# Kernel tuning notes

Hardware: AMD Instinct MI355X
Metric: run time of the kernel (lower is better)

The kernel has to match this reference:

```python
import jax, jax.numpy as jnp
import numpy as np

C_LOGIT = 10.0  # logit clipping constant C from __init__
NEG_INF = -1e9


def setup_inputs() -> dict:
    key = jax.random.key(0)
    ks = jax.random.split(key, 12)
    B, S, E, H = 128, 1024, 128, 128
    sE = 1.0 / np.sqrt(E)
    s2E = 1.0 / np.sqrt(2 * E)
    return {
        "node_context": jnp.zeros((1,), jnp.float32),   # unused: low-decoder results are discarded
        "original_data": jnp.zeros((1,), jnp.float32),  # unused
        "cell_context": jax.random.normal(ks[0], (B, S, E), jnp.float32),
        "high_mask": jnp.zeros((B, S), jnp.float32),
        "low_mask": jnp.zeros((1,), jnp.float32),       # unused
        # learned parameters
        "init_w": jax.random.uniform(ks[1], (2 * E,), jnp.float32, -1.0, 1.0),
        "Wc": jax.random.uniform(ks[2], (E, E), jnp.float32, -sE, sE),    # h_context_embed
        "bc": jax.random.uniform(ks[3], (E,), jnp.float32, -sE, sE),
        "Wv": jax.random.uniform(ks[4], (2 * E, E), jnp.float32, -s2E, s2E),  # v_weight_embed
        "bv": jax.random.uniform(ks[5], (E,), jnp.float32, -s2E, s2E),
        "W_ref": jax.random.uniform(ks[6], (E, H), jnp.float32, -sE, sE),  # pointer target proj
        "W_q": jax.random.uniform(ks[7], (E, H), jnp.float32, -sE, sE),    # pointer query proj
        "v": jax.random.uniform(ks[8], (H,), jnp.float32, -1.0 / np.sqrt(H), 1.0 / np.sqrt(H)),
    }


def reference(node_context, original_data, cell_context, high_mask, low_mask,
              init_w, Wc, bc, Wv, bv, W_ref, W_q, v):
    B, S, E = cell_context.shape
    h_bar = jnp.mean(cell_context, axis=1) @ Wc + bc            # [B, E]
    ref = jnp.einsum('bse,eh->bsh', cell_context, W_ref)        # [B, S, H] (loop-invariant)
    q0 = h_bar + (init_w @ Wv + bv)                             # [B, E]
    mask0 = high_mask.at[:, 0].set(1.0)                         # start node masked
    base_key = jax.random.key(42)

    def step(carry, i):
        query, mask, init_h = carry
        q = query @ W_q                                         # [B, H]
        u = C_LOGIT * jnp.tanh(jnp.einsum('bsh,h->bs', jnp.tanh(ref + q[:, None, :]), v))
        logits = jnp.where(mask > 0, NEG_INF, u)                # [B, S]
        k = jax.random.fold_in(base_key, i)
        idx = jax.random.categorical(k, logits)                 # [B] sampled next node
        logp = jnp.take_along_axis(jax.nn.log_softmax(logits, -1), idx[:, None], 1)[:, 0]
        mask = mask.at[jnp.arange(B), idx].set(1.0)             # Environment.update_state
        h = jnp.take_along_axis(cell_context, idx[:, None, None], 1)[:, 0, :]  # gather emb
        init_h = jnp.where(i == 0, h, init_h)                   # frozen after first step
        query = h_bar + jnp.concatenate([init_h, h], axis=-1) @ Wv + bv
        return (query, mask, init_h), (logp, idx)

    init = (q0, mask0, jnp.zeros((B, E), cell_context.dtype))
    _, (logps, idxs) = jax.lax.scan(step, init, jnp.arange(S - 1))
    # original returns (stack(log_probs, 1), stack(idx, 1))
    return logps.T, idxs.T
```

## Files before the change

### kernel.cpp

```cpp
#include <hip/hip_runtime.h>
#include <hip/hip_bf16.h>
#include <stdint.h>

#pragma clang fp contract(off)

#define Bn 128
#define Sn 1024
#define En 128
#define NSTEP 1023
#define REQ_WS ((size_t)Bn * 128 * Sn * 4)

__device__ __forceinline__ uint2 threefry2x32(uint32_t k0, uint32_t k1,
                                              uint32_t x0, uint32_t x1) {
  uint32_t ks2 = k0 ^ k1 ^ 0x1BD11BDAu;
  x0 += k0; x1 += k1;
#define TFR(r) { x0 += x1; x1 = (x1 << (r)) | (x1 >> (32 - (r))); x1 ^= x0; }
  TFR(13) TFR(15) TFR(26) TFR(6)
  x0 += k1;  x1 += ks2 + 1u;
  TFR(17) TFR(29) TFR(16) TFR(24)
  x0 += ks2; x1 += k0 + 2u;
  TFR(13) TFR(15) TFR(26) TFR(6)
  x0 += k0;  x1 += k1 + 3u;
  TFR(17) TFR(29) TFR(16) TFR(24)
  x0 += k1;  x1 += ks2 + 4u;
  TFR(13) TFR(15) TFR(26) TFR(6)
  x0 += ks2; x1 += k0 + 5u;
#undef TFR
  return make_uint2(x0, x1);
}

__device__ __forceinline__ float xla_tanh(float x) {
#pragma clang fp contract(off)
  float cx = fmaxf(-7.90531110763549805f, fminf(x, 7.90531110763549805f));
  float x2 = cx * cx;
  float nu = -2.76076847742355e-16f;
  nu = x2 * nu + 2.00018790482477e-13f;
  nu = x2 * nu + -8.60467152213735e-11f;
  nu = x2 * nu + 5.12229709037114e-08f;
  nu = x2 * nu + 1.48572235717979e-05f;
  nu = x2 * nu + 6.37261928875436e-04f;
  nu = x2 * nu + 4.89352455891786e-03f;
  nu = cx * nu;
  float de = 1.19825839466702e-06f;
  de = x2 * de + 1.18534705686654e-04f;
  de = x2 * de + 2.26843463243900e-03f;
  de = x2 * de + 4.89352518554385e-03f;
  float r = nu / de;
  return (fabsf(x) < 0.0004f) ? x : r;
}

__device__ __forceinline__ float cephes_logf(float x) {
#pragma clang fp contract(off)
  uint32_t ix = __float_as_uint(x);
  int e = (int)(ix >> 23) - 126;
  float m = __uint_as_float((ix & 0x007FFFFFu) | 0x3F000000u);
  if (m < 0.70710678118654752440f) { e -= 1; m = m + m; }
  float xm = m - 1.0f;
  float z = xm * xm;
  float y = 7.0376836292e-2f;
  y = y * xm + -1.1514610310e-1f;
  y = y * xm + 1.1676998740e-1f;
  y = y * xm + -1.2420140846e-1f;
  y = y * xm + 1.4249322787e-1f;
  y = y * xm + -1.6668057665e-1f;
  y = y * xm + 2.0000714765e-1f;
  y = y * xm + -2.4999993993e-1f;
  y = y * xm + 3.3333331174e-1f;
  y = y * xm;
  y = y * z;
  float fe = (float)e;
  y = y + fe * -2.12194440e-4f;
  y = y - 0.5f * z;
  float res = xm + y;
  res = res + fe * 0.693359375f;
  return res;
}

__device__ __forceinline__ float cephes_expf(float x) {
#pragma clang fp contract(off)
  x = fminf(fmaxf(x, -88.3762626647949f), 88.3762626647950f);
  float fx = x * 1.44269504088896341f + 0.5f;
  fx = floorf(fx);
  x = x - fx * 0.693359375f;
  x = x - fx * -2.12194440e-4f;
  float z = x * x;
  float y = 1.9875691500e-4f;
  y = y * x + 1.3981999507e-3f;
  y = y * x + 8.3334519073e-3f;
  y = y * x + 4.1665795894e-2f;
  y = y * x + 1.6666665459e-1f;
  y = y * x + 5.0000001201e-1f;
  y = y * z + x;
  y = y + 1.0f;
  return ldexpf(y, (int)fx);
}

__device__ __forceinline__ uint32_t f32_orderable(float f) {
  uint32_t b = __float_as_uint(f);
  return (b & 0x80000000u) ? ~b : (b | 0x80000000u);
}

__global__ void k_mark(float* out, float val) { out[0] = val; }

__global__ __launch_bounds__(256) void k_ref(const float* __restrict__ cc,
    const float* __restrict__ W_ref, float* __restrict__ refT) {
#pragma clang fp contract(off)
  int b = blockIdx.y, s0 = blockIdx.x * 128, t = threadIdx.x;
  __shared__ float tile[128 * 129];
  const float* src = cc + ((size_t)b * Sn + s0) * En;
  for (int i = t; i < 128 * 128; i += 256) {
    int sl = i >> 7, e = i & 127;
    tile[sl * 129 + e] = src[i];
  }
  __syncthreads();
  for (int i = t; i < 128 * 128; i += 256) {
    int sl = i >> 7, h = i & 127;
    float acc = 0.0f;
    for (int e = 0; e < En; ++e)
      acc = acc + tile[sl * 129 + e] * W_ref[e * 128 + h];
    refT[((size_t)b * Sn + (s0 + sl)) * 128 + h] = acc;
  }
}

__global__ __launch_bounds__(1024) void k_decode(
    const float* __restrict__ cc, const float* __restrict__ high_mask,
    const float* __restrict__ init_w, const float* __restrict__ Wc,
    const float* __restrict__ bc, const float* __restrict__ Wv,
    const float* __restrict__ bv, const float* __restrict__ W_q,
    const float* __restrict__ v, const float* __restrict__ refT,
    float* __restrict__ out, int half) {
#pragma clang fp contract(off)
  const int b = blockIdx.x, tid = threadIdx.x;
  const int lane = tid & 63, wid = tid >> 6;
  const int hsel = tid & 1;
  const int row1 = tid >> 1;
  __shared__ __align__(16) float wq_s[128 * 128];
  __shared__ __align__(16) float wvhi_s[128 * 128];
  __shared__ __align__(16) float mean_s[128], q_s[128], query_s[128], hbar_s[128];
  __shared__ __align__(16) float v_s[128], bv_s[128], cvec[256], dlow_s[128];
  __shared__ float uv[1024];
  __shared__ unsigned short list2[2][1024];
  __shared__ unsigned long long wkey[16];
  __shared__ float wsum[16];
  __shared__ int n_s;
  __shared__ uint32_t key_s[2];

  for (int j = tid; j < 128 * 128; j += 1024) wq_s[j] = W_q[j];
  for (int j = tid; j < 128 * 128; j += 1024) wvhi_s[j] = Wv[128 * 128 + j];
  if (tid < 128) {
    float acc = 0.0f;
    const float* base = cc + (size_t)b * Sn * En + tid;
    for (int s = 0; s < Sn; ++s) acc = acc + base[(size_t)s * En];
    mean_s[tid] = acc / 1024.0f;
  }
  if (tid == 512) {
    int n = 0;
    for (int s = 0; s < Sn; ++s) {
      bool masked = (s == 0) || (high_mask[(size_t)b * Sn + s] > 0.0f);
      if (!masked) list2[0][n++] = (unsigned short)s;
    }
    n_s = n;
  }
  __syncthreads();
  if (tid < 128) {
    float hb = 0.0f;
    for (int e = 0; e < 128; ++e) hb = hb + mean_s[e] * Wc[e * 128 + tid];
    hb = hb + bc[tid];
    float wd = 0.0f;
    for (int k = 0; k < 256; ++k) wd = wd + init_w[k] * Wv[k * 128 + tid];
    wd = wd + bv[tid];
    hbar_s[tid] = hb;
    query_s[tid] = hb + wd;
    v_s[tid] = v[tid];
    bv_s[tid] = bv[tid];
  }
  __syncthreads();
  const int n0 = n_s;

  const float* refb = refT + (size_t)b * Sn * 128;
  const float4* q4 = (const float4*)q_s;
  const float4* v4 = (const float4*)v_s;

  for (int i = 0; i < NSTEP; ++i) {
    const int n = n0 - i;
    const unsigned short* lcur = list2[i & 1];
    unsigned short* lnxt = list2[(i + 1) & 1];

    if (tid < 128) {
      float acc = 0.0f;
#pragma unroll 8
      for (int k = 0; k < 128; ++k) acc = acc + query_s[k] * wq_s[k * 128 + tid];
      q_s[tid] = acc;
    } else if (tid == 512) {
      uint2 kk2 = threefry2x32(0u, 42u, 0u, (uint32_t)i);
      key_s[0] = kk2.x; key_s[1] = kk2.y;
    }
    __syncthreads();

    const int npass = (2 * n + 1023) >> 10;
    unsigned long long kk = 0ull;
    float ee = 0.0f;
    for (int pass = 0; pass < npass; ++pass) {
      const int row = (pass << 9) + row1;
      if (row < n) {
        const int s = lcur[row];
        const float4* rb4 = (const float4*)(refb + (size_t)s * 128);
        float4 rA[8];
#pragma unroll
        for (int j = 0; j < 8; ++j) rA[j] = rb4[2 * j + hsel];
        float a0 = 0.f, a1 = 0.f, a2 = 0.f, a3 = 0.f;
        float4 rB[8];
#pragma unroll
        for (int c2 = 0; c2 < 8; ++c2) {
          rB[c2] = rb4[2 * (c2 + 8) + hsel];
          const float4 qv = q4[2 * c2 + hsel];
          const float4 vv = v4[2 * c2 + hsel];
          const float4 r = rA[c2];
          a0 = a0 + xla_tanh(r.x + qv.x) * vv.x;
          a1 = a1 + xla_tanh(r.y + qv.y) * vv.y;
          a2 = a2 + xla_tanh(r.z + qv.z) * vv.z;
          a3 = a3 + xla_tanh(r.w + qv.w) * vv.w;
        }
#pragma unroll
        for (int c2 = 8; c2 < 16; ++c2) {
          const float4 qv = q4[2 * c2 + hsel];
          const float4 vv = v4[2 * c2 + hsel];
          const float4 r = rB[c2 - 8];
          a0 = a0 + xla_tanh(r.x + qv.x) * vv.x;
          a1 = a1 + xla_tanh(r.y + qv.y) * vv.y;
          a2 = a2 + xla_tanh(r.z + qv.z) * vv.z;
          a3 = a3 + xla_tanh(r.w + qv.w) * vv.w;
        }
        float o0 = __shfl_xor(a0, 1, 64), o1 = __shfl_xor(a1, 1, 64);
        float o2 = __shfl_xor(a2, 1, 64), o3 = __shfl_xor(a3, 1, 64);
        if (hsel == 0) {
          float h0 = a0 + o0, h1 = a1 + o1, h2 = a2 + o2, h3 = a3 + o3;
          float dot = (h0 + h2) + (h1 + h3);
          float u = 10.0f * xla_tanh(dot);
          uint32_t f = (uint32_t)(b * Sn + s);
          uint2 hh = threefry2x32(key_s[0], key_s[1], 0u, f);
          uint32_t bits = hh.x ^ hh.y;
          float uf = __uint_as_float((bits >> 9) | 0x3F800000u) - 1.0f;
          uf = uf + 1.17549435e-38f;
          uf = fmaxf(1.17549435e-38f, uf);
          float g = -cephes_logf(-cephes_logf(uf));
          float y = u + g;
          uv[row] = u;
          unsigned long long k2 =
              ((unsigned long long)f32_orderable(y) << 32) | (uint32_t)(0xFFFFFFFFu - (uint32_t)row);
          if (k2 > kk) kk = k2;
          ee = ee + cephes_expf(u);
        }
      }
    }
    for (int off = 32; off >= 1; off >>= 1) {
      unsigned long long o = __shfl_xor(kk, off, 64);
      if (o > kk) kk = o;
      ee = ee + __shfl_xor(ee, off, 64);
    }
    if (lane == 0) { wkey[wid] = kk; wsum[wid] = ee; }
    __syncthreads();

    unsigned long long km = wkey[0];
    float es = wsum[0];
    for (int w = 1; w < 16; ++w) {
      if (wkey[w] > km) km = wkey[w];
      es = es + wsum[w];
    }
    int p = (int)(0xFFFFFFFFu - (uint32_t)(km & 0xFFFFFFFFu));
    p = (p >= 0 && p < 1024) ? p : 0;
    const int idx = lcur[p];
    if (tid < 128) {
      float hval = cc[((size_t)b * Sn + idx) * En + tid];
      cvec[128 + tid] = hval;
      if (i == 0) cvec[tid] = hval;
    }
    if (tid < n - 1) lnxt[tid] = lcur[tid + (tid >= p ? 1 : 0)];
    if (tid == 0) {
      float logp = uv[p] - cephes_logf(es);
      out[(size_t)b * NSTEP + i] = logp;
      out[(size_t)half + (size_t)b * NSTEP + i] = (float)idx;
    }
    __syncthreads();

    if (tid < 128) {
      float d;
      if (i == 0) {
        float dl = 0.0f;
#pragma unroll 8
        for (int k = 0; k < 128; ++k) dl = dl + cvec[k] * Wv[k * 128 + tid];
        dlow_s[tid] = dl;
        d = dl;
      } else {
        d = dlow_s[tid];
      }
#pragma unroll 8
      for (int k = 0; k < 128; ++k) d = d + cvec[128 + k] * wvhi_s[k * 128 + tid];
      query_s[tid] = (hbar_s[tid] + d) + bv_s[tid];
    }
    __syncthreads();
  }
}

extern "C" void kernel_launch(void* const* d_in, const int* in_sizes, int n_in,
                              void* d_out, int out_size, void* d_ws, size_t ws_size,
                              hipStream_t stream) {
  const float* cc     = (const float*)d_in[2];
  const float* hm     = (const float*)d_in[3];
  const float* init_w = (const float*)d_in[5];
  const float* Wc     = (const float*)d_in[6];
  const float* bc     = (const float*)d_in[7];
  const float* Wv     = (const float*)d_in[8];
  const float* bv     = (const float*)d_in[9];
  const float* W_ref  = (const float*)d_in[10];
  const float* W_q    = (const float*)d_in[11];
  const float* v      = (const float*)d_in[12];
  float* out = (float*)d_out;

  if (ws_size < REQ_WS) {
    float mib = (float)(ws_size >> 20);
    hipLaunchKernelGGL(k_mark, dim3(1), dim3(1), 0, stream, out, 100000.0f * (mib + 1.0f));
    return;
  }

  float* refT = (float*)d_ws;
  const int half = out_size / 2;

  hipLaunchKernelGGL(k_ref, dim3(Sn / 128, Bn), dim3(256), 0, stream, cc, W_ref, refT);
  hipLaunchKernelGGL(k_decode, dim3(Bn), dim3(1024), 0, stream,
                     cc, hm, init_w, Wc, bc, Wv, bv, W_q, v, refT, out, half);
}
```

Baseline: 22.43 ms.

## Split each batch row's decode across two workgroups with global-memory handshake

```diff
diff --git a/kernel.cpp b/kernel.cpp
--- a/kernel.cpp
+++ b/kernel.cpp
@@ -9,6 +9,8 @@
 #define En 128
 #define NSTEP 1023
 #define REQ_WS ((size_t)Bn * 128 * Sn * 4)
+#define XCH_BYTES 5120
+#define REQ_WS2 (REQ_WS + (size_t)8192)
 
 __device__ __forceinline__ uint2 threefry2x32(uint32_t k0, uint32_t k1,
                                               uint32_t x0, uint32_t x1) {
@@ -102,6 +104,8 @@
 
 __global__ void k_mark(float* out, float val) { out[0] = val; }
 
+__global__ void k_zero(unsigned int* p) { p[blockIdx.x * 256 + threadIdx.x] = 0u; }
+
 __global__ __launch_bounds__(256) void k_ref(const float* __restrict__ cc,
     const float* __restrict__ W_ref, float* __restrict__ refT) {
 #pragma clang fp contract(off)
@@ -122,7 +126,204 @@
   }
 }
 
-__global__ __launch_bounds__(1024) void k_decode(
+__global__ __launch_bounds__(1024) void k_decode2(
+    const float* __restrict__ cc, const float* __restrict__ high_mask,
+    const float* __restrict__ init_w, const float* __restrict__ Wc,
+    const float* __restrict__ bc, const float* __restrict__ Wv,
+    const float* __restrict__ bv, const float* __restrict__ W_q,
+    const float* __restrict__ v, const float* __restrict__ refT,
+    float* __restrict__ out, int half, void* xbase) {
+#pragma clang fp contract(off)
+  const int b = blockIdx.x >> 1, side = blockIdx.x & 1, tid = threadIdx.x;
+  const int lane = tid & 63, wid = tid >> 6;
+  const int hsel = tid & 1;
+  unsigned long long* xk = (unsigned long long*)xbase;
+  float* xe = (float*)((char*)xbase + 2048);
+  float* xu = (float*)((char*)xbase + 3072);
+  uint32_t* xf = (uint32_t*)((char*)xbase + 4096);
+  const int me = (b << 1) | side, other = me ^ 1;
+
+  __shared__ __align__(16) float wq_s[128 * 128];
+  __shared__ __align__(16) float wvhi_s[128 * 128];
+  __shared__ __align__(16) float mean_s[128], q_s[128], query_s[128], hbar_s[128];
+  __shared__ __align__(16) float v_s[128], bv_s[128], cvec[256], dlow_s[128];
+  __shared__ float uv[1024];
+  __shared__ unsigned short list2[2][1024];
+  __shared__ unsigned long long wkey[16];
+  __shared__ float wsum[16];
+  __shared__ int n_s, p_ls;
+  __shared__ float up_ls, es_ls;
+  __shared__ uint32_t key_s[2];
+
+  for (int j = tid; j < 128 * 128; j += 1024) wq_s[j] = W_q[j];
+  for (int j = tid; j < 128 * 128; j += 1024) wvhi_s[j] = Wv[128 * 128 + j];
+  if (tid < 128) {
+    float acc = 0.0f;
+    const float* base = cc + (size_t)b * Sn * En + tid;
+    for (int s = 0; s < Sn; ++s) acc = acc + base[(size_t)s * En];
+    mean_s[tid] = acc / 1024.0f;
+  }
+  if (tid == 512) {
+    int n = 0;
+    for (int s = 0; s < Sn; ++s) {
+      bool masked = (s == 0) || (high_mask[(size_t)b * Sn + s] > 0.0f);
+      if (!masked) list2[0][n++] = (unsigned short)s;
+    }
+    n_s = n;
+  }
+  __syncthreads();
+  if (tid < 128) {
+    float hb = 0.0f;
+    for (int e = 0; e < 128; ++e) hb = hb + mean_s[e] * Wc[e * 128 + tid];
+    hb = hb + bc[tid];
+    float wd = 0.0f;
+    for (int k = 0; k < 256; ++k) wd = wd + init_w[k] * Wv[k * 128 + tid];
+    wd = wd + bv[tid];
+    hbar_s[tid] = hb;
+    query_s[tid] = hb + wd;
+    v_s[tid] = v[tid];
+    bv_s[tid] = bv[tid];
+  }
+  __syncthreads();
+  const int n0 = n_s;
+
+  const float* refb = refT + (size_t)b * Sn * 128;
+  const float4* q4 = (const float4*)q_s;
+  const float4* v4 = (const float4*)v_s;
+
+  for (int i = 0; i < NSTEP; ++i) {
+    const int n = n0 - i;
+    const unsigned short* lcur = list2[i & 1];
+    unsigned short* lnxt = list2[(i + 1) & 1];
+
+    if (tid < 128) {
+      float acc = 0.0f;
+#pragma unroll 8
+      for (int k = 0; k < 128; ++k) acc = acc + query_s[k] * wq_s[k * 128 + tid];
+      q_s[tid] = acc;
+    } else if (tid == 512) {
+      uint2 kk2 = threefry2x32(0u, 42u, 0u, (uint32_t)i);
+      key_s[0] = kk2.x; key_s[1] = kk2.y;
+    }
+    __syncthreads();
+
+    const int row = 2 * (tid >> 1) + side;
+    unsigned long long kk = 0ull;
+    float ee = 0.0f;
+    if (row < n) {
+      const int s = lcur[row];
+      const float4* rb4 = (const float4*)(refb + (size_t)s * 128);
+      float4 rA[8];
+#pragma unroll
+      for (int j = 0; j < 8; ++j) rA[j] = rb4[2 * j + hsel];
+      float a0 = 0.f, a1 = 0.f, a2 = 0.f, a3 = 0.f;
+      float4 rB[8];
+#pragma unroll
+      for (int c2 = 0; c2 < 8; ++c2) {
+        rB[c2] = rb4[2 * (c2 + 8) + hsel];
+        const float4 qv = q4[2 * c2 + hsel];
+        const float4 vv = v4[2 * c2 + hsel];
+        const float4 r = rA[c2];
+        a0 = a0 + xla_tanh(r.x + qv.x) * vv.x;
+        a1 = a1 + xla_tanh(r.y + qv.y) * vv.y;
+        a2 = a2 + xla_tanh(r.z + qv.z) * vv.z;
+        a3 = a3 + xla_tanh(r.w + qv.w) * vv.w;
+      }
+#pragma unroll
+      for (int c2 = 8; c2 < 16; ++c2) {
+        const float4 qv = q4[2 * c2 + hsel];
+        const float4 vv = v4[2 * c2 + hsel];
+        const float4 r = rB[c2 - 8];
+        a0 = a0 + xla_tanh(r.x + qv.x) * vv.x;
+        a1 = a1 + xla_tanh(r.y + qv.y) * vv.y;
+        a2 = a2 + xla_tanh(r.z + qv.z) * vv.z;
+        a3 = a3 + xla_tanh(r.w + qv.w) * vv.w;
+      }
+      float o0 = __shfl_xor(a0, 1, 64), o1 = __shfl_xor(a1, 1, 64);
+      float o2 = __shfl_xor(a2, 1, 64), o3 = __shfl_xor(a3, 1, 64);
+      if (hsel == 0) {
+        float h0 = a0 + o0, h1 = a1 + o1, h2 = a2 + o2, h3 = a3 + o3;
+        float dot = (h0 + h2) + (h1 + h3);
+        float u = 10.0f * xla_tanh(dot);
+        uint32_t f = (uint32_t)(b * Sn + s);
+        uint2 hh = threefry2x32(key_s[0], key_s[1], 0u, f);
+        uint32_t bits = hh.x ^ hh.y;
+        float uf = __uint_as_float((bits >> 9) | 0x3F800000u) - 1.0f;
+        uf = uf + 1.17549435e-38f;
+        uf = fmaxf(1.17549435e-38f, uf);
+        float g = -cephes_logf(-cephes_logf(uf));
+        float y = u + g;
+        uv[row] = u;
+        kk = ((unsigned long long)f32_orderable(y) << 32) | (uint32_t)(0xFFFFFFFFu - (uint32_t)row);
+        ee = cephes_expf(u);
+      }
+    }
+    for (int off = 32; off >= 1; off >>= 1) {
+      unsigned long long o = __shfl_xor(kk, off, 64);
+      if (o > kk) kk = o;
+      ee = ee + __shfl_xor(ee, off, 64);
+    }
+    if (lane == 0) { wkey[wid] = kk; wsum[wid] = ee; }
+    __syncthreads();
+
+    if (tid == 0) {
+      unsigned long long km = wkey[0]; float es = wsum[0];
+      for (int w = 1; w < 16; ++w) { if (wkey[w] > km) km = wkey[w]; es = es + wsum[w]; }
+      int rloc = (int)(0xFFFFFFFFu - (uint32_t)(km & 0xFFFFFFFFu));
+      float ub = (rloc >= 0 && rloc < 1024) ? uv[rloc] : 0.0f;
+      __hip_atomic_store(&xk[me], km, __ATOMIC_RELAXED, __HIP_MEMORY_SCOPE_AGENT);
+      __hip_atomic_store(&xe[me], es, __ATOMIC_RELAXED, __HIP_MEMORY_SCOPE_AGENT);
+      __hip_atomic_store(&xu[me], ub, __ATOMIC_RELAXED, __HIP_MEMORY_SCOPE_AGENT);
+      __hip_atomic_store(&xf[me], (uint32_t)(i + 1), __ATOMIC_RELEASE, __HIP_MEMORY_SCOPE_AGENT);
+      while (__hip_atomic_load(&xf[other], __ATOMIC_ACQUIRE, __HIP_MEMORY_SCOPE_AGENT)
+             < (uint32_t)(i + 1)) {}
+      unsigned long long ok = __hip_atomic_load(&xk[other], __ATOMIC_RELAXED, __HIP_MEMORY_SCOPE_AGENT);
+      float oe = __hip_atomic_load(&xe[other], __ATOMIC_RELAXED, __HIP_MEMORY_SCOPE_AGENT);
+      float ou = __hip_atomic_load(&xu[other], __ATOMIC_RELAXED, __HIP_MEMORY_SCOPE_AGENT);
+      unsigned long long kfin = km; float upick = ub;
+      if (ok > kfin) { kfin = ok; upick = ou; }
+      int p = (int)(0xFFFFFFFFu - (uint32_t)(kfin & 0xFFFFFFFFu));
+      p = (p >= 0 && p < 1024) ? p : 0;
+      p_ls = p;
+      float esum = es + oe;
+      if (side == 0) {
+        float logp = upick - cephes_logf(esum);
+        out[(size_t)b * NSTEP + i] = logp;
+        out[(size_t)half + (size_t)b * NSTEP + i] = (float)lcur[p];
+      }
+    }
+    __syncthreads();
+
+    const int p = p_ls;
+    const int idx = lcur[p];
+    if (tid < 128) {
+      float hval = cc[((size_t)b * Sn + idx) * En + tid];
+      cvec[128 + tid] = hval;
+      if (i == 0) cvec[tid] = hval;
+    }
+    if (tid < n - 1) lnxt[tid] = lcur[tid + (tid >= p ? 1 : 0)];
+    __syncthreads();
+
+    if (tid < 128) {
+      float d;
+      if (i == 0) {
+        float dl = 0.0f;
+#pragma unroll 8
+        for (int k = 0; k < 128; ++k) dl = dl + cvec[k] * Wv[k * 128 + tid];
+        dlow_s[tid] = dl;
+        d = dl;
+      } else {
+        d = dlow_s[tid];
+      }
+#pragma unroll 8
+      for (int k = 0; k < 128; ++k) d = d + cvec[128 + k] * wvhi_s[k * 128 + tid];
+      query_s[tid] = (hbar_s[tid] + d) + bv_s[tid];
+    }
+    __syncthreads();
+  }
+}
+
+__global__ __launch_bounds__(1024) void k_decode1(
     const float* __restrict__ cc, const float* __restrict__ high_mask,
     const float* __restrict__ init_w, const float* __restrict__ Wc,
     const float* __restrict__ bc, const float* __restrict__ Wv,
@@ -327,6 +528,15 @@
   const int half = out_size / 2;
 
   hipLaunchKernelGGL(k_ref, dim3(Sn / 128, Bn), dim3(256), 0, stream, cc, W_ref, refT);
-  hipLaunchKernelGGL(k_decode, dim3(Bn), dim3(1024), 0, stream,
-                     cc, hm, init_w, Wc, bc, Wv, bv, W_q, v, refT, out, half);
-}
+
+  if (ws_size >= REQ_WS2) {
+    void* xbase = (void*)((char*)d_ws + REQ_WS);
+    hipLaunchKernelGGL(k_zero, dim3(XCH_BYTES / 1024), dim3(256), 0, stream,
+                       (unsigned int*)xbase);
+    hipLaunchKernelGGL(k_decode2, dim3(2 * Bn), dim3(1024), 0, stream,
+                       cc, hm, init_w, Wc, bc, Wv, bv, W_q, v, refT, out, half, xbase);
+  } else {
+    hipLaunchKernelGGL(k_decode1, dim3(Bn), dim3(1024), 0, stream,
+                       cc, hm, init_w, Wc, bc, Wv, bv, W_q, v, refT, out, half);
+  }
+}
```

New measurement: 19.21 ms. 14.4% less time.

## Split each batch row across two cooperating blocks with global-memory handshake

Applied to the files above, without the earlier changes.

```diff
diff --git a/kernel.cpp b/kernel.cpp
--- a/kernel.cpp
+++ b/kernel.cpp
@@ -9,6 +9,7 @@
 #define En 128
 #define NSTEP 1023
 #define REQ_WS ((size_t)Bn * 128 * Sn * 4)
+#define REQ_WS2 (REQ_WS + (size_t)8192)
 
 __device__ __forceinline__ uint2 threefry2x32(uint32_t k0, uint32_t k1,
                                               uint32_t x0, uint32_t x1) {
@@ -102,6 +103,8 @@
 
 __global__ void k_mark(float* out, float val) { out[0] = val; }
 
+__global__ void k_zero(unsigned int* p) { p[blockIdx.x * 256 + threadIdx.x] = 0u; }
+
 __global__ __launch_bounds__(256) void k_ref(const float* __restrict__ cc,
     const float* __restrict__ W_ref, float* __restrict__ refT) {
 #pragma clang fp contract(off)
@@ -122,18 +125,23 @@
   }
 }
 
-__global__ __launch_bounds__(1024) void k_decode(
+__global__ __launch_bounds__(1024, 4) void k_decode2(
     const float* __restrict__ cc, const float* __restrict__ high_mask,
     const float* __restrict__ init_w, const float* __restrict__ Wc,
     const float* __restrict__ bc, const float* __restrict__ Wv,
     const float* __restrict__ bv, const float* __restrict__ W_q,
     const float* __restrict__ v, const float* __restrict__ refT,
-    float* __restrict__ out, int half) {
-#pragma clang fp contract(off)
-  const int b = blockIdx.x, tid = threadIdx.x;
+    float* __restrict__ out, int half, void* xbase) {
+#pragma clang fp contract(off)
+  const int b = blockIdx.x >> 1, side = blockIdx.x & 1, tid = threadIdx.x;
   const int lane = tid & 63, wid = tid >> 6;
   const int hsel = tid & 1;
-  const int row1 = tid >> 1;
+  unsigned long long* xk = (unsigned long long*)xbase;
+  float* xe = (float*)((char*)xbase + 2048);
+  float* xu = (float*)((char*)xbase + 3072);
+  uint32_t* xf = (uint32_t*)((char*)xbase + 4096);
+  const int me = (b << 1) | side, other = me ^ 1;
+
   __shared__ __align__(16) float wq_s[128 * 128];
   __shared__ __align__(16) float wvhi_s[128 * 128];
   __shared__ __align__(16) float mean_s[128], q_s[128], query_s[128], hbar_s[128];
@@ -142,7 +150,7 @@
   __shared__ unsigned short list2[2][1024];
   __shared__ unsigned long long wkey[16];
   __shared__ float wsum[16];
-  __shared__ int n_s;
+  __shared__ int n_s, p_ls;
   __shared__ uint32_t key_s[2];
 
   for (int j = tid; j < 128 * 128; j += 1024) wq_s[j] = W_q[j];
@@ -197,11 +205,10 @@
     }
     __syncthreads();
 
-    const int npass = (2 * n + 1023) >> 10;
     unsigned long long kk = 0ull;
     float ee = 0.0f;
-    for (int pass = 0; pass < npass; ++pass) {
-      const int row = (pass << 9) + row1;
+    if (n > 512) {
+      const int row = 2 * (tid >> 1) + side;
       if (row < n) {
         const int s = lcur[row];
         const float4* rb4 = (const float4*)(refb + (size_t)s * 128);
@@ -246,10 +253,51 @@
           float g = -cephes_logf(-cephes_logf(uf));
           float y = u + g;
           uv[row] = u;
-          unsigned long long k2 =
-              ((unsigned long long)f32_orderable(y) << 32) | (uint32_t)(0xFFFFFFFFu - (uint32_t)row);
-          if (k2 > kk) kk = k2;
-          ee = ee + cephes_expf(u);
+          kk = ((unsigned long long)f32_orderable(y) << 32) | (uint32_t)(0xFFFFFFFFu - (uint32_t)row);
+          ee = cephes_expf(u);
+        }
+      }
+    } else {
+      const int row = 2 * (tid >> 2) + side;
+      const int l4 = tid & 3;
+      if (row < n) {
+        const int s = lcur[row];
+        const float* rb = refb + (size_t)s * 128;
+        float rLo[16], rHi[16];
+#pragma unroll
+        for (int c2 = 0; c2 < 8; ++c2) {
+          rLo[c2] = rb[8 * c2 + l4];
+          rHi[c2] = rb[8 * c2 + 4 + l4];
+        }
+        float aLo = 0.f, aHi = 0.f;
+#pragma unroll
+        for (int c2 = 0; c2 < 8; ++c2) {
+          rLo[c2 + 8] = rb[8 * (c2 + 8) + l4];
+          rHi[c2 + 8] = rb[8 * (c2 + 8) + 4 + l4];
+          aLo = aLo + xla_tanh(rLo[c2] + q_s[8 * c2 + l4]) * v_s[8 * c2 + l4];
+          aHi = aHi + xla_tanh(rHi[c2] + q_s[8 * c2 + 4 + l4]) * v_s[8 * c2 + 4 + l4];
+        }
+#pragma unroll
+        for (int c2 = 8; c2 < 16; ++c2) {
+          aLo = aLo + xla_tanh(rLo[c2] + q_s[8 * c2 + l4]) * v_s[8 * c2 + l4];
+          aHi = aHi + xla_tanh(rHi[c2] + q_s[8 * c2 + 4 + l4]) * v_s[8 * c2 + 4 + l4];
+        }
+        float h = aLo + aHi;
+        float t2 = h + __shfl_xor(h, 2, 64);
+        float t1 = t2 + __shfl_xor(t2, 1, 64);
+        if (l4 == 0) {
+          float u = 10.0f * xla_tanh(t1);
+          uint32_t f = (uint32_t)(b * Sn + s);
+          uint2 hh = threefry2x32(key_s[0], key_s[1], 0u, f);
+          uint32_t bits = hh.x ^ hh.y;
+          float uf = __uint_as_float((bits >> 9) | 0x3F800000u) - 1.0f;
+          uf = uf + 1.17549435e-38f;
+          uf = fmaxf(1.17549435e-38f, uf);
+          float g = -cephes_logf(-cephes_logf(uf));
+          float y = u + g;
+          uv[row] = u;
+          kk = ((unsigned long long)f32_orderable(y) << 32) | (uint32_t)(0xFFFFFFFFu - (uint32_t)row);
+          ee = cephes_expf(u);
         }
       }
     }
@@ -261,14 +309,35 @@
     if (lane == 0) { wkey[wid] = kk; wsum[wid] = ee; }
     __syncthreads();
 
-    unsigned long long km = wkey[0];
-    float es = wsum[0];
-    for (int w = 1; w < 16; ++w) {
-      if (wkey[w] > km) km = wkey[w];
-      es = es + wsum[w];
-    }
-    int p = (int)(0xFFFFFFFFu - (uint32_t)(km & 0xFFFFFFFFu));
-    p = (p >= 0 && p < 1024) ? p : 0;
+    if (tid == 0) {
+      unsigned long long km = wkey[0]; float es = wsum[0];
+      for (int w = 1; w < 16; ++w) { if (wkey[w] > km) km = wkey[w]; es = es + wsum[w]; }
+      int rloc = (int)(0xFFFFFFFFu - (uint32_t)(km & 0xFFFFFFFFu));
+      float ub = (rloc >= 0 && rloc < 1024) ? uv[rloc] : 0.0f;
+      __hip_atomic_store(&xk[me], km, __ATOMIC_RELAXED, __HIP_MEMORY_SCOPE_AGENT);
+      __hip_atomic_store(&xe[me], es, __ATOMIC_RELAXED, __HIP_MEMORY_SCOPE_AGENT);
+      __hip_atomic_store(&xu[me], ub, __ATOMIC_RELAXED, __HIP_MEMORY_SCOPE_AGENT);
+      __hip_atomic_store(&xf[me], (uint32_t)(i + 1), __ATOMIC_RELEASE, __HIP_MEMORY_SCOPE_AGENT);
+      while (__hip_atomic_load(&xf[other], __ATOMIC_ACQUIRE, __HIP_MEMORY_SCOPE_AGENT)
+             < (uint32_t)(i + 1)) {}
+      unsigned long long ok = __hip_atomic_load(&xk[other], __ATOMIC_RELAXED, __HIP_MEMORY_SCOPE_AGENT);
+      float oe = __hip_atomic_load(&xe[other], __ATOMIC_RELAXED, __HIP_MEMORY_SCOPE_AGENT);
+      float ou = __hip_atomic_load(&xu[other], __ATOMIC_RELAXED, __HIP_MEMORY_SCOPE_AGENT);
+      unsigned long long kfin = km; float upick = ub;
+      if (ok > kfin) { kfin = ok; upick = ou; }
+      int p = (int)(0xFFFFFFFFu - (uint32_t)(kfin & 0xFFFFFFFFu));
+      p = (p >= 0 && p < 1024) ? p : 0;
+      p_ls = p;
+      float esum = es + oe;
+      if (side == 0) {
+        float logp = upick - cephes_logf(esum);
+        out[(size_t)b * NSTEP + i] = logp;
+        out[(size_t)half + (size_t)b * NSTEP + i] = (float)lcur[p];
+      }
+    }
+    __syncthreads();
+
+    const int p = p_ls;
     const int idx = lcur[p];
     if (tid < 128) {
       float hval = cc[((size_t)b * Sn + idx) * En + tid];
@@ -276,11 +345,6 @@
       if (i == 0) cvec[tid] = hval;
     }
     if (tid < n - 1) lnxt[tid] = lcur[tid + (tid >= p ? 1 : 0)];
-    if (tid == 0) {
-      float logp = uv[p] - cephes_logf(es);
-      out[(size_t)b * NSTEP + i] = logp;
-      out[(size_t)half + (size_t)b * NSTEP + i] = (float)idx;
-    }
     __syncthreads();
 
     if (tid < 128) {
@@ -317,7 +381,7 @@
   const float* v      = (const float*)d_in[12];
   float* out = (float*)d_out;
 
-  if (ws_size < REQ_WS) {
+  if (ws_size < REQ_WS2) {
     float mib = (float)(ws_size >> 20);
     hipLaunchKernelGGL(k_mark, dim3(1), dim3(1), 0, stream, out, 100000.0f * (mib + 1.0f));
     return;
@@ -325,8 +389,10 @@
 
   float* refT = (float*)d_ws;
   const int half = out_size / 2;
+  void* xbase = (void*)((char*)d_ws + REQ_WS);
 
   hipLaunchKernelGGL(k_ref, dim3(Sn / 128, Bn), dim3(256), 0, stream, cc, W_ref, refT);
-  hipLaunchKernelGGL(k_decode, dim3(Bn), dim3(1024), 0, stream,
-                     cc, hm, init_w, Wc, bc, Wv, bv, W_q, v, refT, out, half);
-}
+  hipLaunchKernelGGL(k_zero, dim3(5), dim3(256), 0, stream, (unsigned int*)xbase);
+  hipLaunchKernelGGL(k_decode2, dim3(2 * Bn), dim3(1024), 0, stream,
+                     cc, hm, init_w, Wc, bc, Wv, bv, W_q, v, refT, out, half, xbase);
+}
```

Result: faster. 19.06 ms (-15.0%).
